# Optimization experiments

Measured on AMD Instinct MI355X. Metric: run time of the kernel, lower is better.

The kernel has to match this reference:

```python
import jax, jax.numpy as jnp
from jax import lax
import numpy as np

IN, FC1, H = 12, 32, 16  # hard-coded dims from the module

def setup_inputs() -> dict:
    key = jax.random.key(0)
    ks = jax.random.split(key, 12)
    B, T = 4096, 512
    s = 0.1
    return {
        "x":   jax.random.normal(ks[0], (B, T, IN), dtype=jnp.float32),
        "h0":  jax.random.normal(ks[1], (1, B, H), dtype=jnp.float32),
        "c0":  jax.random.normal(ks[2], (1, B, H), dtype=jnp.float32),
        "W1":  jax.random.normal(ks[3], (FC1, IN), dtype=jnp.float32) * s,
        "b1":  jax.random.normal(ks[4], (FC1,), dtype=jnp.float32) * s,
        "W_ih": jax.random.normal(ks[5], (4 * H, FC1), dtype=jnp.float32) * s,
        "W_hh": jax.random.normal(ks[6], (4 * H, H), dtype=jnp.float32) * s,
        "b_ih": jax.random.normal(ks[7], (4 * H,), dtype=jnp.float32) * s,
        "b_hh": jax.random.normal(ks[8], (4 * H,), dtype=jnp.float32) * s,
        "W2":  jax.random.normal(ks[9], (1, H), dtype=jnp.float32) * s,
        "b2":  jax.random.normal(ks[10], (1,), dtype=jnp.float32) * s,
    }

def reference(x, h0, c0, W1, b1, W_ih, W_hh, b_ih, b_hh, W2, b2):
    # fc1 + ReLU: [B,T,12] -> [B,T,32]
    u = jnp.maximum(jnp.einsum('bti,fi->btf', x, W1) + b1, 0.0)
    # Precompute input contribution to all gates: [B,T,4H]
    xg = jnp.einsum('btf,gf->btg', u, W_ih) + (b_ih + b_hh)
    def step(carry, xg_t):
        ht, ct = carry  # [B,H]
        gates = xg_t + ht @ W_hh.T  # [B,4H]; PyTorch gate order i,f,g,o
        i, f, g, o = jnp.split(gates, 4, axis=-1)
        ct = jax.nn.sigmoid(f) * ct + jax.nn.sigmoid(i) * jnp.tanh(g)
        ht = jax.nn.sigmoid(o) * jnp.tanh(ct)
        return (ht, ct), None
    (hT, cT), _ = lax.scan(step, (h0[0], c0[0]), xg.transpose(1, 0, 2))
    # last_step of batch_first LSTM output == final hidden state hT
    out = jnp.tanh(hT @ W2.T + b2)  # [B,1]
    return out, hT[None], cT[None]
```

## Files before the change

kernel.cpp:

```cpp
#include <hip/hip_runtime.h>

typedef __fp16 f16;
typedef __attribute__((ext_vector_type(4))) __fp16 h16x4;
typedef __attribute__((ext_vector_type(4))) float f32x4;

__device__ __forceinline__ float sigm(float x) {
    return __builtin_amdgcn_rcpf(1.0f + __expf(-x));
}
__device__ __forceinline__ float tanh_fast(float x) {
    return 1.0f - 2.0f * __builtin_amdgcn_rcpf(1.0f + __expf(2.0f * x));
}
__device__ __forceinline__ h16x4 cvt4(float4 v) {
    h16x4 r; r[0] = (f16)v.x; r[1] = (f16)v.y; r[2] = (f16)v.z; r[3] = (f16)v.w;
    return r;
}
__device__ __forceinline__ h16x4 pack4(float a, float b, float c, float d) {
    auto p0 = __builtin_amdgcn_cvt_pkrtz(a, b);
    auto p1 = __builtin_amdgcn_cvt_pkrtz(c, d);
    uint2 u = make_uint2(__builtin_bit_cast(unsigned, p0),
                         __builtin_bit_cast(unsigned, p1));
    return __builtin_bit_cast(h16x4, u);
}
__device__ __forceinline__ float sel4(f32x4 v, bool q1, bool q2) {
    float a = q1 ? v[1] : v[0];
    float b = q1 ? v[3] : v[2];
    return q2 ? b : a;
}

__global__ __launch_bounds__(128) void reflex_fused(
    const float* __restrict__ x,
    const float* __restrict__ h0, const float* __restrict__ c0,
    const float* __restrict__ W1, const float* __restrict__ b1,
    const float* __restrict__ Wih, const float* __restrict__ Whh,
    const float* __restrict__ bih, const float* __restrict__ bhh,
    const float* __restrict__ W2, const float* __restrict__ b2,
    float* __restrict__ dout)
{
    const int tid = threadIdx.x;
    const int lane = tid & 63;
    const int m = lane & 15, hi = lane >> 4;
    const int b0 = blockIdx.x << 2;

    __shared__ f32x4 xgl[2][1024];

    if (tid >= 64) {
        const int e = m & 3, q = m >> 2;
        const int b = b0 + e;
        h16x4 a1[2]; f32x4 c1[2];
#pragma unroll
        for (int nt = 0; nt < 2; ++nt) {
            float4 wv = make_float4(0.f, 0.f, 0.f, 0.f);
            if (hi < 3) wv = *(const float4*)(W1 + (nt * 16 + m) * 12 + 4 * hi);
            a1[nt] = cvt4(wv);
            float4 bv = *(const float4*)(b1 + nt * 16 + 4 * hi);
            c1[nt] = f32x4{bv.x, bv.y, bv.z, bv.w};
        }
        h16x4 a2[4][2]; f32x4 cbp[4];
#pragma unroll
        for (int G = 0; G < 4; ++G) {
            const int gr = G * 16 + m;
#pragma unroll
            for (int s = 0; s < 2; ++s)
                a2[G][s] = cvt4(*(const float4*)(Wih + gr * 32 + s * 16 + 4 * hi));
            float4 bi = *(const float4*)(bih + G * 16 + 4 * hi);
            float4 bh = *(const float4*)(bhh + G * 16 + 4 * hi);
            cbp[G] = f32x4{bi.x + bh.x, bi.y + bh.y, bi.z + bh.z, bi.w + bh.w};
        }
        f32x4* pst0 = &xgl[0][q * 64 + hi * 4 + e];
        f32x4* pst1 = &xgl[1][q * 64 + hi * 4 + e];
        const float* xp = x + ((size_t)b * 512 + q) * 12 + 4 * hi;
        float4 BXA[4], BXB[4];

#define LOADT(BX) do {                                                         \
    if (hi < 3) {                                                              \
        BX[0] = *(const float4*)(xp);                                          \
        BX[1] = *(const float4*)(xp + 48);                                     \
        BX[2] = *(const float4*)(xp + 96);                                     \
        BX[3] = *(const float4*)(xp + 144);                                    \
    }                                                                          \
    xp += 192;                                                                 \
} while (0)

#define GENSLICE(PST, BXV, CC) do {                                            \
    h16x4 bx = {0, 0, 0, 0};                                                   \
    if (hi < 3) bx = cvt4(BXV);                                                \
    f32x4 d0 = __builtin_amdgcn_mfma_f32_16x16x16f16(a1[0], bx, c1[0],0,0,0);  \
    f32x4 d1 = __builtin_amdgcn_mfma_f32_16x16x16f16(a1[1], bx, c1[1],0,0,0);  \
    h16x4 u0 = pack4(fmaxf(d0[0],0.f), fmaxf(d0[1],0.f),                       \
                     fmaxf(d0[2],0.f), fmaxf(d0[3],0.f));                      \
    h16x4 u1 = pack4(fmaxf(d1[0],0.f), fmaxf(d1[1],0.f),                       \
                     fmaxf(d1[2],0.f), fmaxf(d1[3],0.f));                      \
    f32x4 A0 = __builtin_amdgcn_mfma_f32_16x16x16f16(a2[0][0], u0, cbp[0],0,0,0);\
    f32x4 A1 = __builtin_amdgcn_mfma_f32_16x16x16f16(a2[1][0], u0, cbp[1],0,0,0);\
    f32x4 A2 = __builtin_amdgcn_mfma_f32_16x16x16f16(a2[2][0], u0, cbp[2],0,0,0);\
    f32x4 A3 = __builtin_amdgcn_mfma_f32_16x16x16f16(a2[3][0], u0, cbp[3],0,0,0);\
    A0 = __builtin_amdgcn_mfma_f32_16x16x16f16(a2[0][1], u1, A0, 0, 0, 0);     \
    A1 = __builtin_amdgcn_mfma_f32_16x16x16f16(a2[1][1], u1, A1, 0, 0, 0);     \
    A2 = __builtin_amdgcn_mfma_f32_16x16x16f16(a2[2][1], u1, A2, 0, 0, 0);     \
    A3 = __builtin_amdgcn_mfma_f32_16x16x16f16(a2[3][1], u1, A3, 0, 0, 0);     \
    (PST)[(CC) * 256 +  0] = A0;                                               \
    (PST)[(CC) * 256 + 16] = A1;                                               \
    (PST)[(CC) * 256 + 32] = A2;                                               \
    (PST)[(CC) * 256 + 48] = A3;                                               \
} while (0)

#define GENT(PST, BX) do {                                                     \
    GENSLICE(PST, BX[0], 0); GENSLICE(PST, BX[1], 1);                          \
    GENSLICE(PST, BX[2], 2); GENSLICE(PST, BX[3], 3);                          \
} while (0)

        LOADT(BXA);
        for (int F2 = 0; F2 < 16; ++F2) {
            LOADT(BXB);
            GENT(pst0, BXA);
            __syncthreads();
            if (F2 < 15) LOADT(BXA);
            GENT(pst1, BXB);
            __syncthreads();
        }
#undef LOADT
#undef GENSLICE
#undef GENT
    } else {
        const int e = m >> 2, q = m & 3;
        const int b = b0 + e;
        const bool q1 = (q & 1) != 0, q2 = (q & 2) != 0;

        h16x4 ar[4];
#pragma unroll
        for (int G = 0; G < 4; ++G)
            ar[G] = cvt4(*(const float4*)(Whh + (G * 16 + m) * 16 + 4 * hi));
        h16x4 hf = cvt4(*(const float4*)(h0 + b * 16 + 4 * hi));
        float cs = c0[b * 16 + 4 * hi + q];
        float hn = 0.f;
        const f32x4* ldsr = &xgl[0][0];
        const int vbi = hi * 4 + e;

#define STEP(TT, CF, OFF) do {                                                 \
    f32x4 di = __builtin_amdgcn_mfma_f32_16x16x16f16(ar[0], hf, CF[0],0,0,0);  \
    f32x4 df = __builtin_amdgcn_mfma_f32_16x16x16f16(ar[1], hf, CF[1],0,0,0);  \
    f32x4 dg = __builtin_amdgcn_mfma_f32_16x16x16f16(ar[2], hf, CF[2],0,0,0);  \
    f32x4 dq = __builtin_amdgcn_mfma_f32_16x16x16f16(ar[3], hf, CF[3],0,0,0);  \
    if ((TT) < 14) {                                                           \
        CF[0] = ldsr[(OFF) + ((TT) + 2) * 64 +  0 + vbi];                      \
        CF[1] = ldsr[(OFF) + ((TT) + 2) * 64 + 16 + vbi];                      \
        CF[2] = ldsr[(OFF) + ((TT) + 2) * 64 + 32 + vbi];                      \
        CF[3] = ldsr[(OFF) + ((TT) + 2) * 64 + 48 + vbi];                      \
    }                                                                          \
    float gg = sel4(dg, q1, q2); float gi = sel4(di, q1, q2);                  \
    float gf = sel4(df, q1, q2); float go = sel4(dq, q1, q2);                  \
    float tg = tanh_fast(gg);                                                  \
    cs = fmaf(sigm(gf), cs, sigm(gi) * tg);                                    \
    hn = sigm(go) * tanh_fast(cs);                                             \
    int hnb = __builtin_bit_cast(int, hn);                                     \
    float j0 = __builtin_bit_cast(float,                                       \
        __builtin_amdgcn_mov_dpp(hnb, 0x00, 0xF, 0xF, true));                  \
    float j1 = __builtin_bit_cast(float,                                       \
        __builtin_amdgcn_mov_dpp(hnb, 0x55, 0xF, 0xF, true));                  \
    float j2 = __builtin_bit_cast(float,                                       \
        __builtin_amdgcn_mov_dpp(hnb, 0xAA, 0xF, 0xF, true));                  \
    float j3 = __builtin_bit_cast(float,                                       \
        __builtin_amdgcn_mov_dpp(hnb, 0xFF, 0xF, 0xF, true));                  \
    hf = pack4(j0, j1, j2, j3);                                                \
} while (0)

#define TILEBODY(OFF) do {                                                     \
    f32x4 CA[4], CB[4];                                                        \
    CA[0] = ldsr[(OFF) +  0 + vbi]; CA[1] = ldsr[(OFF) + 16 + vbi];            \
    CA[2] = ldsr[(OFF) + 32 + vbi]; CA[3] = ldsr[(OFF) + 48 + vbi];            \
    CB[0] = ldsr[(OFF) + 64 + vbi]; CB[1] = ldsr[(OFF) + 80 + vbi];            \
    CB[2] = ldsr[(OFF) + 96 + vbi]; CB[3] = ldsr[(OFF) + 112 + vbi];           \
    STEP(0, CA, OFF);  STEP(1, CB, OFF);                                       \
    STEP(2, CA, OFF);  STEP(3, CB, OFF);                                       \
    STEP(4, CA, OFF);  STEP(5, CB, OFF);                                       \
    STEP(6, CA, OFF);  STEP(7, CB, OFF);                                       \
    STEP(8, CA, OFF);  STEP(9, CB, OFF);                                       \
    STEP(10, CA, OFF); STEP(11, CB, OFF);                                      \
    STEP(12, CA, OFF); STEP(13, CB, OFF);                                      \
    STEP(14, CA, OFF); STEP(15, CB, OFF);                                      \
} while (0)

        __builtin_amdgcn_s_setprio(1);
        for (int T2 = 0; T2 < 16; ++T2) {
            __syncthreads();
            TILEBODY(0);
            __syncthreads();
            TILEBODY(1024);
        }
        __builtin_amdgcn_s_setprio(0);
#undef STEP
#undef TILEBODY

        dout[4096 + b * 16 + 4 * hi + q]         = hn;
        dout[4096 + 65536 + b * 16 + 4 * hi + q] = cs;
        float p = hn * W2[4 * hi + q];
        p += __shfl_xor(p, 1);
        p += __shfl_xor(p, 2);
        p += __shfl_xor(p, 16);
        p += __shfl_xor(p, 32);
        if (hi == 0 && q == 0) dout[b0 + e] = tanh_fast(p + b2[0]);
    }
}

extern "C" void kernel_launch(void* const* d_in, const int* in_sizes, int n_in,
                              void* d_out, int out_size, void* d_ws, size_t ws_size,
                              hipStream_t stream)
{
    const float* x   = (const float*)d_in[0];
    const float* h0  = (const float*)d_in[1];
    const float* c0  = (const float*)d_in[2];
    const float* W1  = (const float*)d_in[3];
    const float* b1  = (const float*)d_in[4];
    const float* Wih = (const float*)d_in[5];
    const float* Whh = (const float*)d_in[6];
    const float* bih = (const float*)d_in[7];
    const float* bhh = (const float*)d_in[8];
    const float* W2  = (const float*)d_in[9];
    const float* b2  = (const float*)d_in[10];
    float* out = (float*)d_out;

    reflex_fused<<<dim3(1024), dim3(128), 0, stream>>>(
        x, h0, c0, W1, b1, Wih, Whh, bih, bhh, W2, b2, out);
}
```

Before: 101.9 us.

## Pack eight batch rows per block, two hidden units per lane in LSTM recurrence

Each block now handles 8 batch rows instead of 4, and the grid is halved to 512 blocks. The MFMA N dimension is filled with 8 batches by 2 timesteps in the producer and 8 batches in the recurrence. Each recurrence lane now computes two hidden units, and h is redistributed with a single DPP swap plus selects instead of four DPP broadcasts. The aim is to cut per-step shuffle overhead and make better use of MFMA columns. In exchange, each lane does twice the serial activation math, fewer waves are in flight, and the producer runs twice as many sync iterations.

```diff
diff --git a/kernel.cpp b/kernel.cpp
--- a/kernel.cpp
+++ b/kernel.cpp
@@ -20,11 +20,6 @@
     uint2 u = make_uint2(__builtin_bit_cast(unsigned, p0),
                          __builtin_bit_cast(unsigned, p1));
     return __builtin_bit_cast(h16x4, u);
-}
-__device__ __forceinline__ float sel4(f32x4 v, bool q1, bool q2) {
-    float a = q1 ? v[1] : v[0];
-    float b = q1 ? v[3] : v[2];
-    return q2 ? b : a;
 }
 
 __global__ __launch_bounds__(128) void reflex_fused(
@@ -39,13 +34,13 @@
     const int tid = threadIdx.x;
     const int lane = tid & 63;
     const int m = lane & 15, hi = lane >> 4;
-    const int b0 = blockIdx.x << 2;
+    const int b0 = blockIdx.x << 3;
 
     __shared__ f32x4 xgl[2][1024];
 
     if (tid >= 64) {
-        const int e = m & 3, q = m >> 2;
-        const int b = b0 + e;
+        const int pe = m & 7, ts = m >> 3;
+        const int b = b0 + pe;
         h16x4 a1[2]; f32x4 c1[2];
 #pragma unroll
         for (int nt = 0; nt < 2; ++nt) {
@@ -66,19 +61,18 @@
             float4 bh = *(const float4*)(bhh + G * 16 + 4 * hi);
             cbp[G] = f32x4{bi.x + bh.x, bi.y + bh.y, bi.z + bh.z, bi.w + bh.w};
         }
-        f32x4* pst0 = &xgl[0][q * 64 + hi * 4 + e];
-        f32x4* pst1 = &xgl[1][q * 64 + hi * 4 + e];
-        const float* xp = x + ((size_t)b * 512 + q) * 12 + 4 * hi;
+        f32x4* pst0 = &xgl[0][ts * 128 + hi * 8 + pe];
+        f32x4* pst1 = &xgl[1][ts * 128 + hi * 8 + pe];
+        const float* xp = x + ((size_t)b * 512 + ts) * 12 + 4 * hi;
         float4 BXA[4], BXB[4];
 
-#define LOADT(BX) do {                                                         \
+#define LOADT(BX, TILE) do {                                                   \
     if (hi < 3) {                                                              \
-        BX[0] = *(const float4*)(xp);                                          \
-        BX[1] = *(const float4*)(xp + 48);                                     \
-        BX[2] = *(const float4*)(xp + 96);                                     \
-        BX[3] = *(const float4*)(xp + 144);                                    \
+        BX[0] = *(const float4*)(xp + ((TILE) * 8 + 0) * 12);                  \
+        BX[1] = *(const float4*)(xp + ((TILE) * 8 + 2) * 12);                  \
+        BX[2] = *(const float4*)(xp + ((TILE) * 8 + 4) * 12);                  \
+        BX[3] = *(const float4*)(xp + ((TILE) * 8 + 6) * 12);                  \
     }                                                                          \
-    xp += 192;                                                                 \
 } while (0)
 
 #define GENSLICE(PST, BXV, CC) do {                                            \
@@ -99,9 +93,9 @@
     A2 = __builtin_amdgcn_mfma_f32_16x16x16f16(a2[2][1], u1, A2, 0, 0, 0);     \
     A3 = __builtin_amdgcn_mfma_f32_16x16x16f16(a2[3][1], u1, A3, 0, 0, 0);     \
     (PST)[(CC) * 256 +  0] = A0;                                               \
-    (PST)[(CC) * 256 + 16] = A1;                                               \
-    (PST)[(CC) * 256 + 32] = A2;                                               \
-    (PST)[(CC) * 256 + 48] = A3;                                               \
+    (PST)[(CC) * 256 + 32] = A1;                                               \
+    (PST)[(CC) * 256 + 64] = A2;                                               \
+    (PST)[(CC) * 256 + 96] = A3;                                               \
 } while (0)
 
 #define GENT(PST, BX) do {                                                     \
@@ -109,12 +103,12 @@
     GENSLICE(PST, BX[2], 2); GENSLICE(PST, BX[3], 3);                          \
 } while (0)
 
-        LOADT(BXA);
-        for (int F2 = 0; F2 < 16; ++F2) {
-            LOADT(BXB);
+        LOADT(BXA, 0);
+        for (int F2 = 0; F2 < 32; ++F2) {
+            LOADT(BXB, 2 * F2 + 1);
             GENT(pst0, BXA);
             __syncthreads();
-            if (F2 < 15) LOADT(BXA);
+            if (F2 < 31) LOADT(BXA, 2 * F2 + 2);
             GENT(pst1, BXB);
             __syncthreads();
         }
@@ -122,66 +116,63 @@
 #undef GENSLICE
 #undef GENT
     } else {
-        const int e = m >> 2, q = m & 3;
-        const int b = b0 + e;
-        const bool q1 = (q & 1) != 0, q2 = (q & 2) != 0;
+        const int ce = m >> 1, p = m & 1;
+        const int b = b0 + ce;
 
         h16x4 ar[4];
 #pragma unroll
         for (int G = 0; G < 4; ++G)
             ar[G] = cvt4(*(const float4*)(Whh + (G * 16 + m) * 16 + 4 * hi));
         h16x4 hf = cvt4(*(const float4*)(h0 + b * 16 + 4 * hi));
-        float cs = c0[b * 16 + 4 * hi + q];
-        float hn = 0.f;
+        float2 cc = *(const float2*)(c0 + b * 16 + 4 * hi + 2 * p);
+        float cs0 = cc.x, cs1 = cc.y;
+        float hn0 = 0.f, hn1 = 0.f;
         const f32x4* ldsr = &xgl[0][0];
-        const int vbi = hi * 4 + e;
+        const int vbi = hi * 8 + ce;
 
 #define STEP(TT, CF, OFF) do {                                                 \
     f32x4 di = __builtin_amdgcn_mfma_f32_16x16x16f16(ar[0], hf, CF[0],0,0,0);  \
     f32x4 df = __builtin_amdgcn_mfma_f32_16x16x16f16(ar[1], hf, CF[1],0,0,0);  \
     f32x4 dg = __builtin_amdgcn_mfma_f32_16x16x16f16(ar[2], hf, CF[2],0,0,0);  \
     f32x4 dq = __builtin_amdgcn_mfma_f32_16x16x16f16(ar[3], hf, CF[3],0,0,0);  \
-    if ((TT) < 14) {                                                           \
-        CF[0] = ldsr[(OFF) + ((TT) + 2) * 64 +  0 + vbi];                      \
-        CF[1] = ldsr[(OFF) + ((TT) + 2) * 64 + 16 + vbi];                      \
-        CF[2] = ldsr[(OFF) + ((TT) + 2) * 64 + 32 + vbi];                      \
-        CF[3] = ldsr[(OFF) + ((TT) + 2) * 64 + 48 + vbi];                      \
+    if ((TT) < 6) {                                                            \
+        CF[0] = ldsr[(OFF) + ((TT) + 2) * 128 +  0 + vbi];                     \
+        CF[1] = ldsr[(OFF) + ((TT) + 2) * 128 + 32 + vbi];                     \
+        CF[2] = ldsr[(OFF) + ((TT) + 2) * 128 + 64 + vbi];                     \
+        CF[3] = ldsr[(OFF) + ((TT) + 2) * 128 + 96 + vbi];                     \
     }                                                                          \
-    float gg = sel4(dg, q1, q2); float gi = sel4(di, q1, q2);                  \
-    float gf = sel4(df, q1, q2); float go = sel4(dq, q1, q2);                  \
-    float tg = tanh_fast(gg);                                                  \
-    cs = fmaf(sigm(gf), cs, sigm(gi) * tg);                                    \
-    hn = sigm(go) * tanh_fast(cs);                                             \
-    int hnb = __builtin_bit_cast(int, hn);                                     \
-    float j0 = __builtin_bit_cast(float,                                       \
-        __builtin_amdgcn_mov_dpp(hnb, 0x00, 0xF, 0xF, true));                  \
-    float j1 = __builtin_bit_cast(float,                                       \
-        __builtin_amdgcn_mov_dpp(hnb, 0x55, 0xF, 0xF, true));                  \
-    float j2 = __builtin_bit_cast(float,                                       \
-        __builtin_amdgcn_mov_dpp(hnb, 0xAA, 0xF, 0xF, true));                  \
-    float j3 = __builtin_bit_cast(float,                                       \
-        __builtin_amdgcn_mov_dpp(hnb, 0xFF, 0xF, 0xF, true));                  \
-    hf = pack4(j0, j1, j2, j3);                                                \
+    float i0 = p ? di[2] : di[0], i1 = p ? di[3] : di[1];                      \
+    float f0 = p ? df[2] : df[0], f1 = p ? df[3] : df[1];                      \
+    float g0 = p ? dg[2] : dg[0], g1 = p ? dg[3] : dg[1];                      \
+    float o0 = p ? dq[2] : dq[0], o1 = p ? dq[3] : dq[1];                      \
+    float tg0 = tanh_fast(g0), tg1 = tanh_fast(g1);                            \
+    cs0 = fmaf(sigm(f0), cs0, sigm(i0) * tg0);                                 \
+    cs1 = fmaf(sigm(f1), cs1, sigm(i1) * tg1);                                 \
+    hn0 = sigm(o0) * tanh_fast(cs0);                                           \
+    hn1 = sigm(o1) * tanh_fast(cs1);                                           \
+    auto pk = __builtin_amdgcn_cvt_pkrtz(hn0, hn1);                            \
+    unsigned wown = __builtin_bit_cast(unsigned, pk);                          \
+    unsigned woth = (unsigned)__builtin_amdgcn_mov_dpp(                        \
+        (int)wown, 0xB1, 0xF, 0xF, true);                                      \
+    unsigned w0 = p ? woth : wown;                                             \
+    unsigned w1 = p ? wown : woth;                                             \
+    hf = __builtin_bit_cast(h16x4, make_uint2(w0, w1));                        \
 } while (0)
 
 #define TILEBODY(OFF) do {                                                     \
     f32x4 CA[4], CB[4];                                                        \
-    CA[0] = ldsr[(OFF) +  0 + vbi]; CA[1] = ldsr[(OFF) + 16 + vbi];            \
-    CA[2] = ldsr[(OFF) + 32 + vbi]; CA[3] = ldsr[(OFF) + 48 + vbi];            \
-    CB[0] = ldsr[(OFF) + 64 + vbi]; CB[1] = ldsr[(OFF) + 80 + vbi];            \
-    CB[2] = ldsr[(OFF) + 96 + vbi]; CB[3] = ldsr[(OFF) + 112 + vbi];           \
-    STEP(0, CA, OFF);  STEP(1, CB, OFF);                                       \
-    STEP(2, CA, OFF);  STEP(3, CB, OFF);                                       \
-    STEP(4, CA, OFF);  STEP(5, CB, OFF);                                       \
-    STEP(6, CA, OFF);  STEP(7, CB, OFF);                                       \
-    STEP(8, CA, OFF);  STEP(9, CB, OFF);                                       \
-    STEP(10, CA, OFF); STEP(11, CB, OFF);                                      \
-    STEP(12, CA, OFF); STEP(13, CB, OFF);                                      \
-    STEP(14, CA, OFF); STEP(15, CB, OFF);                                      \
+    CA[0] = ldsr[(OFF) +   0 + vbi]; CA[1] = ldsr[(OFF) +  32 + vbi];          \
+    CA[2] = ldsr[(OFF) +  64 + vbi]; CA[3] = ldsr[(OFF) +  96 + vbi];          \
+    CB[0] = ldsr[(OFF) + 128 + vbi]; CB[1] = ldsr[(OFF) + 160 + vbi];          \
+    CB[2] = ldsr[(OFF) + 192 + vbi]; CB[3] = ldsr[(OFF) + 224 + vbi];          \
+    STEP(0, CA, OFF); STEP(1, CB, OFF);                                        \
+    STEP(2, CA, OFF); STEP(3, CB, OFF);                                        \
+    STEP(4, CA, OFF); STEP(5, CB, OFF);                                        \
+    STEP(6, CA, OFF); STEP(7, CB, OFF);                                        \
 } while (0)
 
         __builtin_amdgcn_s_setprio(1);
-        for (int T2 = 0; T2 < 16; ++T2) {
+        for (int T2 = 0; T2 < 32; ++T2) {
             __syncthreads();
             TILEBODY(0);
             __syncthreads();
@@ -191,14 +182,15 @@
 #undef STEP
 #undef TILEBODY
 
-        dout[4096 + b * 16 + 4 * hi + q]         = hn;
-        dout[4096 + 65536 + b * 16 + 4 * hi + q] = cs;
-        float p = hn * W2[4 * hi + q];
-        p += __shfl_xor(p, 1);
-        p += __shfl_xor(p, 2);
-        p += __shfl_xor(p, 16);
-        p += __shfl_xor(p, 32);
-        if (hi == 0 && q == 0) dout[b0 + e] = tanh_fast(p + b2[0]);
+        const int ho = 4 * hi + 2 * p;
+        *(float2*)(dout + 4096 + b * 16 + ho)         = make_float2(hn0, hn1);
+        *(float2*)(dout + 4096 + 65536 + b * 16 + ho) = make_float2(cs0, cs1);
+        float2 w2v = *(const float2*)(W2 + ho);
+        float pl = hn0 * w2v.x + hn1 * w2v.y;
+        pl += __shfl_xor(pl, 1);
+        pl += __shfl_xor(pl, 16);
+        pl += __shfl_xor(pl, 32);
+        if (p == 0 && hi == 0) dout[b0 + ce] = tanh_fast(pl + b2[0]);
     }
 }
 
@@ -219,6 +211,6 @@
     const float* b2  = (const float*)d_in[10];
     float* out = (float*)d_out;
 
-    reflex_fused<<<dim3(1024), dim3(128), 0, stream>>>(
+    reflex_fused<<<dim3(512), dim3(128), 0, stream>>>(
         x, h0, c0, W1, b1, Wih, Whh, bih, bhh, W2, b2, out);
 }
```

After: 124.7 us. +22.4%, slower.
